# Kernel optimization log

Measured on AMD Instinct MI355X. Metric: run time of the kernel, lower is better.

## Reference

```python
import jax, jax.numpy as jnp
import numpy as np

K = 7            # neighbor volumes (NNN heads)
PS = 10          # patch size
ADJ = PS // 2    # patch anchor offset (use_adj)
WOFF = 29 // 2   # search window half-size (ws=29)
KSEARCH = 224    # hardcoded in forward
T, C, E, HH, WW = 1, 8, 8, 64, 64


def _box1(a, axis):
    # sliding-window sum of length PS anchored at i-ADJ, zero outside
    pw = [(0, 0)] * a.ndim
    pw[axis] = (ADJ, PS - 1 - ADJ)
    ap = jnp.pad(a, pw)
    c = jnp.cumsum(ap, axis=axis)
    zp = [(0, 0)] * a.ndim
    zp[axis] = (1, 0)
    c = jnp.pad(c, zp)
    n = a.shape[axis]
    return jax.lax.slice_in_dim(c, PS, PS + n, axis=axis) - jax.lax.slice_in_dim(c, 0, n, axis=axis)


def box_sum(a):
    return _box1(_box1(a, -2), -1)


def setup_inputs():
    key = jax.random.key(0)
    ks = jax.random.split(key, 5)
    x = jax.random.normal(ks[0], (T, C, HH, WW), jnp.float32)
    xe = jax.random.normal(ks[1], (T, E, HH, WW), jnp.float32)
    ye = jax.random.normal(ks[2], (T, E, HH, WW), jnp.float32)
    y = jax.random.normal(ks[3], (T, C, HH, WW), jnp.float32)
    log_temp = 0.1 * jax.random.normal(ks[4], (T, 1, HH, WW), jnp.float32)
    return {"x": x, "xe": xe, "ye": ye, "y": y, "log_temp": log_temp}


def reference(x, xe, ye, y, log_temp):
    pad = lambda a: jnp.pad(a, ((0, 0), (0, 0), (1, 1), (1, 1)))
    x, xe, ye, y, log_temp = pad(x), pad(xe), pad(ye), pad(y), pad(log_temp)
    H, W = x.shape[-2:]
    Q = H * W
    xe0, ye0 = xe[0], ye[0]
    # search window offsets (ws x ws)
    dy, dx = np.meshgrid(np.arange(-WOFF, WOFF + 1), np.arange(-WOFF, WOFF + 1), indexing='ij')
    dy = jnp.asarray(dy.ravel()); dx = jnp.asarray(dx.ravel())
    nW = dy.shape[0]  # 841
    # patch squared norms (zero padded patches)
    n2_q = box_sum((ye0 ** 2).sum(0))   # (H,W)
    n2_db = box_sum((xe0 ** 2).sum(0))  # (H,W)
    xep = jnp.pad(xe0, ((0, 0), (WOFF, WOFF), (WOFF, WOFF)))
    n2p = jnp.pad(n2_db, WOFF)
    def shifted(d):
        s = jax.lax.dynamic_slice(xep, (0, WOFF + d[0], WOFF + d[1]), (E, H, W))
        n = jax.lax.dynamic_slice(n2p, (WOFF + d[0], WOFF + d[1]), (H, W))
        return s, n
    xe_s, n2_s = jax.vmap(shifted)(jnp.stack([dy, dx], -1))  # (nW,E,H,W),(nW,H,W)
    cross = box_sum((ye0[None] * xe_s).sum(1))               # (nW,H,W)
    dist = n2_q[None] + n2_s - 2.0 * cross                   # L2^2, (nW,H,W)
    qy = jnp.arange(H)[:, None]; qx = jnp.arange(W)[None, :]
    valid = ((qy[None] + dy[:, None, None] >= 0) & (qy[None] + dy[:, None, None] < H)
             & (qx[None] + dx[:, None, None] >= 0) & (qx[None] + dx[:, None, None] < W))
    self_m = (dy == 0) & (dx == 0)  # remove_self
    dist = jnp.where(valid & ~self_m[:, None, None], dist, 1e10)
    dist = dist.transpose(1, 2, 0).reshape(Q, nW)
    negd, idx = jax.lax.top_k(-dist, KSEARCH)  # closest KSEARCH, negd = -L2
    # avg-pooled log temperature per query patch
    lt = (box_sum(log_temp[0, 0]) / (PS * PS)).reshape(Q)
    # NeuralNearestNeighbors: iterative continuous top-k relaxation
    logits = negd / jnp.exp(lt)[:, None]
    Ws = []
    for _ in range(K):
        w = jax.nn.softmax(logits, axis=-1)
        logits = logits + jnp.log(jnp.clip(1.0 - w, 1e-6, None))
        Ws.append(w)
    Wk = jnp.stack(Ws)  # (K,Q,KSEARCH)
    # absolute candidate coords
    qyf = jnp.repeat(jnp.arange(H), W); qxf = jnp.tile(jnp.arange(W), H)
    ny = qyf[:, None] + dy[idx]; nx = qxf[:, None] + dx[idx]  # (Q,KSEARCH)
    # weighted patch sum (gather per patch offset)
    xpad = jnp.pad(x[0], ((0, 0), (ADJ, PS - 1 - ADJ), (ADJ, PS - 1 - ADJ)))
    z = jnp.zeros((K, Q, C, PS, PS), x.dtype)
    for oy in range(PS):
        for ox in range(PS):
            vals = xpad[:, ny + oy, nx + ox]  # (C,Q,KSEARCH)
            z = z.at[:, :, :, oy, ox].set(jnp.einsum('kqj,cqj->kqc', Wk, vals))
    # fold with counting (iFoldz): overlap-add of patches + coverage counts
    zp = z.transpose(1, 0, 2, 3, 4).reshape(H, W, K * C, PS, PS)
    buf = jnp.zeros((K * C, H + PS - 1, W + PS - 1), x.dtype)
    cnt = jnp.zeros((H + PS - 1, W + PS - 1), x.dtype)
    for oy in range(PS):
        for ox in range(PS):
            buf = buf.at[:, oy:oy + H, ox:ox + W].add(zp[:, :, :, oy, ox].transpose(2, 0, 1))
            cnt = cnt.at[oy:oy + H, ox:ox + W].add(1.0)
    vid = buf[:, ADJ:ADJ + H, ADJ:ADJ + W]
    zvid = cnt[ADJ:ADJ + H, ADJ:ADJ + W]
    zagg = vid / zvid[None]
    zagg = zagg.reshape(T, K, C, H, W) - y.reshape(T, 1, C, H, W)
    zagg = zagg.reshape(T, K * C, H, W)
    out = jnp.concatenate([y, zagg], axis=1)[..., 1:-1, 1:-1]
    return out
```

## Files before the change

kernel.cpp:

```cpp
#include <hip/hip_runtime.h>
#include <hip/hip_bf16.h>

#define HP    66
#define QTOT  (HP*HP)
#define NWIN  29
#define NW    (NWIN*NWIN)
#define KK    7
#define WOFF2 14
#define NZ    15
#define QB    8
#define QBN   545
#define NIT   27
#define NSEG3 198
#define PSTR  4368


__global__ __launch_bounds__(256) void k_prep1(const float* __restrict__ x,
    const float* __restrict__ xe, const float* __restrict__ ye,
    const float* __restrict__ lt, float* __restrict__ ws) {
  int p = blockIdx.x * 256 + threadIdx.x;
  if (p >= QTOT) return;
  int i = p / HP, j = p % HP;
  bool in = (i >= 1 && i < HP-1 && j >= 1 && j < HP-1);
  int src = (i-1)*64 + (j-1);
  float vy[8], vx[8], vv[8];
  float sy = 0.f, sx = 0.f;
#pragma unroll
  for (int e = 0; e < 8; ++e) {
    vy[e] = in ? ye[e*4096 + src] : 0.f;
    vx[e] = in ? xe[e*4096 + src] : 0.f;
    vv[e] = in ? x [e*4096 + src] : 0.f;
    sy += vy[e]*vy[e]; sx += vx[e]*vx[e];
  }
  float4* yp = (float4*)(ws + (size_t)p*8);
  float4* xp = (float4*)(ws + 8*QTOT + (size_t)p*8);
  yp[0] = make_float4(vy[0], vy[1], vy[2], vy[3]);
  yp[1] = make_float4(vy[4], vy[5], vy[6], vy[7]);
  xp[0] = make_float4(vx[0], vx[1], vx[2], vx[3]);
  xp[1] = make_float4(vx[4], vx[5], vx[6], vx[7]);
  unsigned wd[4];
#pragma unroll
  for (int e2 = 0; e2 < 4; ++e2) {
    unsigned lo = __bfloat16_as_ushort(__float2bfloat16(vv[2*e2]));
    unsigned hi = __bfloat16_as_ushort(__float2bfloat16(vv[2*e2+1]));
    wd[e2] = lo | (hi << 16);
  }
  uint4* xb = (uint4*)(ws + 16*QTOT);
  uint4 v4; v4.x = wd[0]; v4.y = wd[1]; v4.z = wd[2]; v4.w = wd[3];
  xb[p] = v4;
  ws[24*QTOT + p] = sy;
  ws[25*QTOT + p] = sx;
  ws[26*QTOT + p] = in ? lt[src] : 0.f;
}

__global__ __launch_bounds__(256) void k_prep2(float* __restrict__ ws) {
  int p = blockIdx.x * 256 + threadIdx.x;
  if (p >= QTOT) return;
  int i = p / HP, j = p % HP;
  const float* sqye = ws + 24*QTOT;
  const float* sqxe = ws + 25*QTOT;
  const float* lt66 = ws + 26*QTOT;
  float a = 0.f, b = 0.f, c = 0.f;
  for (int u = -5; u <= 4; ++u) {
    int ii = i + u; if (ii < 0 || ii >= HP) continue;
    for (int v = -5; v <= 4; ++v) {
      int jj = j + v; if (jj < 0 || jj >= HP) continue;
      int o = ii*HP + jj;
      a += sqye[o]; b += sqxe[o]; c += lt66[o];
    }
  }
  ws[27*QTOT + p] = a;
  ws[28*QTOT + p] = b;
  ws[29*QTOT + p] = c * 0.01f;
}

__global__ __launch_bounds__(256) void k_dist(const float* __restrict__ ws,
                                              float* __restrict__ dist) {
  __shared__ float4 s4[QTOT/4];
  __shared__ float h[QTOT];
  float* s = (float*)s4;
  int w = blockIdx.x, tid = threadIdx.x;
  int dy = w / NWIN - WOFF2, dx = w % NWIN - WOFF2;
  const float* yex = ws;
  const float* xex = ws + 8*QTOT;
  const float* n2q  = ws + 27*QTOT;
  const float* n2db = ws + 28*QTOT;
  for (int p = tid; p < QTOT; p += 256) {
    int i = p / HP, j = p % HP;
    int ii = i + dy, jj = j + dx;
    float sv = 0.f;
    if (ii >= 0 && ii < HP && jj >= 0 && jj < HP) {
      int p2 = ii*HP + jj;
      const float4* yp = (const float4*)(yex + (size_t)p*8);
      const float4* xp = (const float4*)(xex + (size_t)p2*8);
      float4 a0 = yp[0], a1 = yp[1], b0 = xp[0], b1 = xp[1];
      sv += a0.x*b0.x; sv += a0.y*b0.y; sv += a0.z*b0.z; sv += a0.w*b0.w;
      sv += a1.x*b1.x; sv += a1.y*b1.y; sv += a1.z*b1.z; sv += a1.w*b1.w;
    }
    s[p] = sv;
  }
  __syncthreads();
  if (tid < NSEG3) {
    int row = tid % HP, seg = tid / HP, c0 = seg*22;
    const float* ar = s + row*HP;
    float* hr = h + row*HP;
    float w9[9]; float sum = 0.f;
#pragma unroll
    for (int t = 0; t < 9; ++t) {
      int jj = c0 - 5 + t;
      float v = (jj >= 0) ? ar[jj] : 0.f;
      w9[t] = v; sum += v;
    }
#pragma unroll
    for (int t = 0; t < 22; ++t) {
      int j = c0 + t, jn = j + 4;
      float nv = (jn < HP) ? ar[jn] : 0.f;
      sum += nv;
      hr[j] = sum;
      sum -= w9[t % 9];
      w9[t % 9] = nv;
    }
  }
  __syncthreads();
  if (tid < NSEG3) {
    int col = tid % HP, seg = tid / HP, r0 = seg*22;
    float w9[9]; float sum = 0.f;
#pragma unroll
    for (int t = 0; t < 9; ++t) {
      int ii = r0 - 5 + t;
      float v = (ii >= 0) ? h[ii*HP + col] : 0.f;
      w9[t] = v; sum += v;
    }
#pragma unroll
    for (int t = 0; t < 22; ++t) {
      int i = r0 + t, in2 = i + 4;
      float nv = (in2 < HP) ? h[in2*HP + col] : 0.f;
      sum += nv;
      float cr = sum;
      int p = i*HP + col;
      int ii = i + dy, jj = col + dx;
      bool valid = (ii >= 0 && ii < HP && jj >= 0 && jj < HP);
      float dv = 1e10f;
      if (valid && !(dy == 0 && dx == 0))
        dv = n2q[p] + n2db[ii*HP + jj] - 2.f * cr;
      s[p] = dv;
      sum -= w9[t % 9];
      w9[t % 9] = nv;
    }
  }
  __syncthreads();
  float4* dq = (float4*)(dist + (size_t)w*QTOT);
  for (int p4 = tid; p4 < QTOT/4; p4 += 256)
    dq[p4] = s4[p4];
}

__global__ __launch_bounds__(256) void k_weights(const float* __restrict__ ws,
    const float* __restrict__ dist, __hip_bfloat16* __restrict__ wf) {
  __shared__ float mh[32], sh[32];
  int tid = threadIdx.x;
  int bid = blockIdx.x;
  int xcd = bid & 7, idx = bid >> 3;
  int qb = (xcd == 0) ? idx : (69 + (xcd-1)*68 + idx);
  int qq = tid & (QB-1);
  int q = qb * QB + qq;
  bool qok = q < QTOT;
  int qs = qok ? q : (QTOT - 1);
  int wg = tid >> 3;
  int wave = tid >> 6;
  float invT = __expf(-ws[29*QTOT + qs]);
  float lv[NIT];
#pragma unroll
  for (int it = 0; it < NIT; ++it) {
    int w = wg + it*32;
    lv[it] = (qok && w < NW) ? (-dist[w*QTOT + qs] * invT) : -3.0e38f;
  }
  for (int k = 0; k < KK; ++k) {
    float pm = -3.0e38f;
#pragma unroll
    for (int it = 0; it < NIT; ++it) pm = fmaxf(pm, lv[it]);
    pm = fmaxf(pm, __shfl_xor(pm, 8, 64));
    pm = fmaxf(pm, __shfl_xor(pm, 16, 64));
    pm = fmaxf(pm, __shfl_xor(pm, 32, 64));
    if ((tid & 63) < QB) mh[wave*QB + qq] = pm;
    __syncthreads();
    float m = fmaxf(fmaxf(mh[qq], mh[QB+qq]), fmaxf(mh[2*QB+qq], mh[3*QB+qq]));
    float psum = 0.f;
#pragma unroll
    for (int it = 0; it < NIT; ++it) psum += __expf(lv[it] - m);
    psum += __shfl_xor(psum, 8, 64);
    psum += __shfl_xor(psum, 16, 64);
    psum += __shfl_xor(psum, 32, 64);
    if ((tid & 63) < QB) sh[wave*QB + qq] = psum;
    __syncthreads();
    float invden = 1.0f / (sh[qq] + sh[QB+qq] + sh[2*QB+qq] + sh[3*QB+qq]);
    size_t kbase = (size_t)k*NW*PSTR + q;
#pragma unroll
    for (int it = 0; it < NIT; ++it) {
      int w = wg + it*32;
      if (qok && w < NW) {
        float wgt = __expf(lv[it] - m) * invden;
        wf[kbase + (size_t)w*PSTR] = __float2bfloat16(wgt);
        if (k < KK-1 && wgt > 1e-9f)
          lv[it] += __logf(fmaxf(1.f - wgt, 1e-6f));
      }
    }
    __syncthreads();
  }
}

__global__ __launch_bounds__(256) void k_boxw(__hip_bfloat16* __restrict__ wfp) {
  __shared__ uint4 au4[546];
  __shared__ uint4 hu4[546];
  int bid = blockIdx.x;
  uint4* plane = (uint4*)(wfp + (size_t)bid*PSTR);
  int tid = threadIdx.x;
  for (int qb = tid; qb < 546; qb += 256)
    au4[qb] = plane[qb];
  __syncthreads();
  const unsigned short* a16 = (const unsigned short*)au4;
  unsigned short* h16 = (unsigned short*)hu4;
  for (int task = tid; task < 396; task += 256) {
    int row = task % HP, seg = task / HP, c0 = seg*11;
    const unsigned short* ar = a16 + row*HP;
    unsigned short* hr = h16 + row*HP;
    float w9[9]; float sum = 0.f;
#pragma unroll
    for (int t = 0; t < 9; ++t) {
      int jj = c0 - 4 + t;
      float v = (jj >= 0) ? __uint_as_float((unsigned)ar[jj] << 16) : 0.f;
      w9[t] = v; sum += v;
    }
#pragma unroll
    for (int t = 0; t < 11; ++t) {
      int j = c0 + t, jn = j + 5;
      float nv = (jn < HP) ? __uint_as_float((unsigned)ar[jn] << 16) : 0.f;
      sum += nv;
      hr[j] = __bfloat16_as_ushort(__float2bfloat16(sum));
      sum -= w9[t % 9];
      w9[t % 9] = nv;
    }
  }
  __syncthreads();
  unsigned short* a16w = (unsigned short*)au4;
  for (int task = tid; task < 396; task += 256) {
    int col = task % HP, seg = task / HP, r0 = seg*11;
    float w9[9]; float sum = 0.f;
#pragma unroll
    for (int t = 0; t < 9; ++t) {
      int ii = r0 - 4 + t;
      float v = (ii >= 0) ? __uint_as_float((unsigned)h16[ii*HP + col] << 16) : 0.f;
      w9[t] = v; sum += v;
    }
#pragma unroll
    for (int t = 0; t < 11; ++t) {
      int i = r0 + t, in2 = i + 5;
      float nv = (in2 < HP) ? __uint_as_float((unsigned)h16[in2*HP + col] << 16) : 0.f;
      sum += nv;
      a16w[i*HP + col] = __bfloat16_as_ushort(__float2bfloat16(sum));
      sum -= w9[t % 9];
      w9[t % 9] = nv;
    }
  }
  __syncthreads();
  for (int qb = tid; qb < 546; qb += 256)
    plane[qb] = au4[qb];
}

__global__ __launch_bounds__(256) void k_contract(const float* __restrict__ ws,
    const unsigned short* __restrict__ wfb, float* __restrict__ accb2) {
  __shared__ uint4 xt4[17][45];
  int t = blockIdx.x, z = blockIdx.y, k = blockIdx.z, tid = threadIdx.x;
  int I0 = (t >> 2) * 16, J0 = (t & 3) * 16;
  int dylo = -WOFF2 + 2*z;
  int gy0 = I0 + 1 + dylo, gx0 = J0 - 13;
  const uint4* xb = (const uint4*)(ws + 16*QTOT);
  for (int idx = tid; idx < 17*44; idx += 256) {
    int r = idx / 44, cc = idx % 44;
    int gy = gy0 + r, gx = gx0 + cc;
    uint4 v = make_uint4(0u, 0u, 0u, 0u);
    if (gy >= 0 && gy < HP && gx >= 0 && gx < HP) v = xb[gy*HP + gx];
    xt4[r][cc] = v;
  }
  __syncthreads();
  int il = tid >> 4, jl = tid & 15;
  int I = I0 + 1 + il, J = J0 + 1 + jl;
  int pix = I*HP + J;
  float acc[8];
#pragma unroll
  for (int c = 0; c < 8; ++c) acc[c] = 0.f;
  int ndd = (z == NZ-1) ? 1 : 2;
  for (int dd = 0; dd < ndd; ++dd) {
    int wrow = (dylo + dd + WOFF2) * NWIN;
    const unsigned short* wp = wfb + ((size_t)k*NW + wrow)*PSTR + pix;
    unsigned short wv[NWIN];
#pragma unroll
    for (int dxw = 0; dxw < NWIN; ++dxw) wv[dxw] = wp[(size_t)dxw*PSTR];
    int r = il + dd;
#pragma unroll
    for (int dxw = 0; dxw < NWIN; ++dxw) {
      float wgt = __uint_as_float((unsigned)wv[dxw] << 16);
      uint4 xv = xt4[r][jl + dxw];
      acc[0] += wgt * __uint_as_float(xv.x << 16);
      acc[1] += wgt * __uint_as_float(xv.x & 0xffff0000u);
      acc[2] += wgt * __uint_as_float(xv.y << 16);
      acc[3] += wgt * __uint_as_float(xv.y & 0xffff0000u);
      acc[4] += wgt * __uint_as_float(xv.z << 16);
      acc[5] += wgt * __uint_as_float(xv.z & 0xffff0000u);
      acc[6] += wgt * __uint_as_float(xv.w << 16);
      acc[7] += wgt * __uint_as_float(xv.w & 0xffff0000u);
    }
  }
  int px64 = (I-1)*64 + (J-1);
#pragma unroll
  for (int c = 0; c < 8; ++c)
    accb2[((z*56 + k*8 + c)*4096) + px64] = acc[c];
}

__global__ __launch_bounds__(256) void k_final(const float* __restrict__ y,
    const float* __restrict__ accb2, float* __restrict__ out) {
  int idx = blockIdx.x * 256 + threadIdx.x;
  int ch = idx >> 12, px = idx & 4095;
  if (ch < 8) { out[idx] = y[ch*4096 + px]; return; }
  int kc = ch - 8, c = kc & 7;
  int i = px >> 6, j = px & 63;
  int I = i + 1, J = j + 1;
  int cy = min(I+5, HP-1) - max(I-4, 0) + 1;
  int cx = min(J+5, HP-1) - max(J-4, 0) + 1;
  float s = 0.f;
#pragma unroll
  for (int z = 0; z < NZ; ++z) s += accb2[(z*56 + kc)*4096 + px];
  out[idx] = s / (float)(cy*cx) - y[c*4096 + px];
}

extern "C" void kernel_launch(void* const* d_in, const int* in_sizes, int n_in,
                              void* d_out, int out_size, void* d_ws, size_t ws_size,
                              hipStream_t stream) {
  const float* x  = (const float*)d_in[0];
  const float* xe = (const float*)d_in[1];
  const float* ye = (const float*)d_in[2];
  const float* y  = (const float*)d_in[3];
  const float* lt = (const float*)d_in[4];
  float* ws   = (float*)d_ws;
  float* dist = ws + 30*QTOT;
  __hip_bfloat16* wf = (__hip_bfloat16*)(dist + (size_t)NW*QTOT);
  float* accb2 = dist;
  float* out = (float*)d_out;

  k_prep1<<<(QTOT + 255)/256, 256, 0, stream>>>(x, xe, ye, lt, ws);
  k_prep2<<<(QTOT + 255)/256, 256, 0, stream>>>(ws);
  k_dist<<<NW, 256, 0, stream>>>(ws, dist);
  k_weights<<<QBN, 256, 0, stream>>>(ws, dist, wf);
  k_boxw<<<KK*NW, 256, 0, stream>>>(wf);
  k_contract<<<dim3(16, NZ, KK), 256, 0, stream>>>(ws, (const unsigned short*)wf, accb2);
  k_final<<<out_size/256, 256, 0, stream>>>(y, accb2, out);
}
```

Before: 157.2 us.

## Fuse weight box filtering into contraction kernel with per-dy tiles

Removes the separate box-filter kernel over all weight planes and instead computes the 10x10 box sum on the fly inside the contraction, loading a 25x25 halo tile of each weight plane into shared memory per dx offset. The grid now covers every dy row separately, so the final reduction sums 29 partial buffers instead of 15. This avoids one full read-modify-write pass over the large bf16 weight buffer, at the cost of redundant halo loads, three barriers per dx step, and a larger partial-sum buffer. Box sums are now kept in fp32 rather than rounded to bf16.

```diff
diff --git a/kernel.cpp b/kernel.cpp
--- a/kernel.cpp
+++ b/kernel.cpp
@@ -7,7 +7,7 @@
 #define NW    (NWIN*NWIN)
 #define KK    7
 #define WOFF2 14
-#define NZ    15
+#define NDY   29
 #define QB    8
 #define QBN   545
 #define NIT   27
@@ -208,112 +208,64 @@
   }
 }
 
-__global__ __launch_bounds__(256) void k_boxw(__hip_bfloat16* __restrict__ wfp) {
-  __shared__ uint4 au4[546];
-  __shared__ uint4 hu4[546];
-  int bid = blockIdx.x;
-  uint4* plane = (uint4*)(wfp + (size_t)bid*PSTR);
-  int tid = threadIdx.x;
-  for (int qb = tid; qb < 546; qb += 256)
-    au4[qb] = plane[qb];
-  __syncthreads();
-  const unsigned short* a16 = (const unsigned short*)au4;
-  unsigned short* h16 = (unsigned short*)hu4;
-  for (int task = tid; task < 396; task += 256) {
-    int row = task % HP, seg = task / HP, c0 = seg*11;
-    const unsigned short* ar = a16 + row*HP;
-    unsigned short* hr = h16 + row*HP;
-    float w9[9]; float sum = 0.f;
-#pragma unroll
-    for (int t = 0; t < 9; ++t) {
-      int jj = c0 - 4 + t;
-      float v = (jj >= 0) ? __uint_as_float((unsigned)ar[jj] << 16) : 0.f;
-      w9[t] = v; sum += v;
-    }
-#pragma unroll
-    for (int t = 0; t < 11; ++t) {
-      int j = c0 + t, jn = j + 5;
-      float nv = (jn < HP) ? __uint_as_float((unsigned)ar[jn] << 16) : 0.f;
-      sum += nv;
-      hr[j] = __bfloat16_as_ushort(__float2bfloat16(sum));
-      sum -= w9[t % 9];
-      w9[t % 9] = nv;
-    }
-  }
-  __syncthreads();
-  unsigned short* a16w = (unsigned short*)au4;
-  for (int task = tid; task < 396; task += 256) {
-    int col = task % HP, seg = task / HP, r0 = seg*11;
-    float w9[9]; float sum = 0.f;
-#pragma unroll
-    for (int t = 0; t < 9; ++t) {
-      int ii = r0 - 4 + t;
-      float v = (ii >= 0) ? __uint_as_float((unsigned)h16[ii*HP + col] << 16) : 0.f;
-      w9[t] = v; sum += v;
-    }
-#pragma unroll
-    for (int t = 0; t < 11; ++t) {
-      int i = r0 + t, in2 = i + 5;
-      float nv = (in2 < HP) ? __uint_as_float((unsigned)h16[in2*HP + col] << 16) : 0.f;
-      sum += nv;
-      a16w[i*HP + col] = __bfloat16_as_ushort(__float2bfloat16(sum));
-      sum -= w9[t % 9];
-      w9[t % 9] = nv;
-    }
-  }
-  __syncthreads();
-  for (int qb = tid; qb < 546; qb += 256)
-    plane[qb] = au4[qb];
-}
-
-__global__ __launch_bounds__(256) void k_contract(const float* __restrict__ ws,
-    const unsigned short* __restrict__ wfb, float* __restrict__ accb2) {
-  __shared__ uint4 xt4[17][45];
-  int t = blockIdx.x, z = blockIdx.y, k = blockIdx.z, tid = threadIdx.x;
+__global__ __launch_bounds__(256) void k_bc(const float* __restrict__ ws,
+    const unsigned short* __restrict__ wf, float* __restrict__ accb2) {
+  __shared__ unsigned short raw[25][26];
+  __shared__ float h[16][26];
+  __shared__ uint4 xt4[16][45];
+  int t = blockIdx.x, dy = blockIdx.y, k = blockIdx.z, tid = threadIdx.x;
+  int dyw = dy - WOFF2;
   int I0 = (t >> 2) * 16, J0 = (t & 3) * 16;
-  int dylo = -WOFF2 + 2*z;
-  int gy0 = I0 + 1 + dylo, gx0 = J0 - 13;
   const uint4* xb = (const uint4*)(ws + 16*QTOT);
-  for (int idx = tid; idx < 17*44; idx += 256) {
+  for (int idx = tid; idx < 16*44; idx += 256) {
     int r = idx / 44, cc = idx % 44;
-    int gy = gy0 + r, gx = gx0 + cc;
+    int gy = I0 + 1 + dyw + r, gx = J0 - 13 + cc;
     uint4 v = make_uint4(0u, 0u, 0u, 0u);
     if (gy >= 0 && gy < HP && gx >= 0 && gx < HP) v = xb[gy*HP + gx];
     xt4[r][cc] = v;
   }
-  __syncthreads();
   int il = tid >> 4, jl = tid & 15;
   int I = I0 + 1 + il, J = J0 + 1 + jl;
-  int pix = I*HP + J;
   float acc[8];
 #pragma unroll
   for (int c = 0; c < 8; ++c) acc[c] = 0.f;
-  int ndd = (z == NZ-1) ? 1 : 2;
-  for (int dd = 0; dd < ndd; ++dd) {
-    int wrow = (dylo + dd + WOFF2) * NWIN;
-    const unsigned short* wp = wfb + ((size_t)k*NW + wrow)*PSTR + pix;
-    unsigned short wv[NWIN];
-#pragma unroll
-    for (int dxw = 0; dxw < NWIN; ++dxw) wv[dxw] = wp[(size_t)dxw*PSTR];
-    int r = il + dd;
-#pragma unroll
-    for (int dxw = 0; dxw < NWIN; ++dxw) {
-      float wgt = __uint_as_float((unsigned)wv[dxw] << 16);
-      uint4 xv = xt4[r][jl + dxw];
-      acc[0] += wgt * __uint_as_float(xv.x << 16);
-      acc[1] += wgt * __uint_as_float(xv.x & 0xffff0000u);
-      acc[2] += wgt * __uint_as_float(xv.y << 16);
-      acc[3] += wgt * __uint_as_float(xv.y & 0xffff0000u);
-      acc[4] += wgt * __uint_as_float(xv.z << 16);
-      acc[5] += wgt * __uint_as_float(xv.z & 0xffff0000u);
-      acc[6] += wgt * __uint_as_float(xv.w << 16);
-      acc[7] += wgt * __uint_as_float(xv.w & 0xffff0000u);
-    }
+  for (int dxw = 0; dxw < NWIN; ++dxw) {
+    const unsigned short* pl = wf + ((size_t)k*NW + dy*NWIN + dxw)*PSTR;
+    for (int s = tid; s < 625; s += 256) {
+      int r = s / 25, cc = s % 25;
+      int gy = I0 - 3 + r, gx = J0 - 3 + cc;
+      unsigned short v = 0;
+      if (gy >= 0 && gy < HP && gx >= 0 && gx < HP) v = pl[gy*HP + gx];
+      raw[r][cc] = v;
+    }
+    __syncthreads();
+    for (int s = tid; s < 400; s += 256) {
+      int r = s % 25, j = s / 25;
+      float sum = 0.f;
+#pragma unroll
+      for (int v = 0; v < 10; ++v)
+        sum += __uint_as_float((unsigned)raw[r][j+v] << 16);
+      h[j][r] = sum;
+    }
+    __syncthreads();
+    float bx = 0.f;
+#pragma unroll
+    for (int u = 0; u < 10; ++u) bx += h[jl][il + u];
+    uint4 xv = xt4[il][jl + dxw];
+    acc[0] += bx * __uint_as_float(xv.x << 16);
+    acc[1] += bx * __uint_as_float(xv.x & 0xffff0000u);
+    acc[2] += bx * __uint_as_float(xv.y << 16);
+    acc[3] += bx * __uint_as_float(xv.y & 0xffff0000u);
+    acc[4] += bx * __uint_as_float(xv.z << 16);
+    acc[5] += bx * __uint_as_float(xv.z & 0xffff0000u);
+    acc[6] += bx * __uint_as_float(xv.w << 16);
+    acc[7] += bx * __uint_as_float(xv.w & 0xffff0000u);
+    __syncthreads();
   }
   int px64 = (I-1)*64 + (J-1);
 #pragma unroll
   for (int c = 0; c < 8; ++c)
-    accb2[((z*56 + k*8 + c)*4096) + px64] = acc[c];
+    accb2[(((size_t)dy*56 + k*8 + c)*4096) + px64] = acc[c];
 }
 
 __global__ __launch_bounds__(256) void k_final(const float* __restrict__ y,
@@ -327,8 +279,8 @@
   int cy = min(I+5, HP-1) - max(I-4, 0) + 1;
   int cx = min(J+5, HP-1) - max(J-4, 0) + 1;
   float s = 0.f;
-#pragma unroll
-  for (int z = 0; z < NZ; ++z) s += accb2[(z*56 + kc)*4096 + px];
+  for (int dy = 0; dy < NDY; ++dy)
+    s += accb2[(((size_t)dy*56 + kc)*4096) + px];
   out[idx] = s / (float)(cy*cx) - y[c*4096 + px];
 }
 
@@ -343,14 +295,13 @@
   float* ws   = (float*)d_ws;
   float* dist = ws + 30*QTOT;
   __hip_bfloat16* wf = (__hip_bfloat16*)(dist + (size_t)NW*QTOT);
-  float* accb2 = dist;
+  float* accb2 = (float*)(wf + (size_t)KK*NW*PSTR);
   float* out = (float*)d_out;
 
   k_prep1<<<(QTOT + 255)/256, 256, 0, stream>>>(x, xe, ye, lt, ws);
   k_prep2<<<(QTOT + 255)/256, 256, 0, stream>>>(ws);
   k_dist<<<NW, 256, 0, stream>>>(ws, dist);
   k_weights<<<QBN, 256, 0, stream>>>(ws, dist, wf);
-  k_boxw<<<KK*NW, 256, 0, stream>>>(wf);
-  k_contract<<<dim3(16, NZ, KK), 256, 0, stream>>>(ws, (const unsigned short*)wf, accb2);
+  k_bc<<<dim3(16, NDY, KK), 256, 0, stream>>>(ws, (const unsigned short*)wf, accb2);
   k_final<<<out_size/256, 256, 0, stream>>>(y, accb2, out);
 }
```

After: 213.6 us. +35.9%, slower.
